# Kernel tuning notes

Hardware: AMD Instinct MI355X
Metric: run time of the kernel (lower is better)

Reference implementation:

```python
import jax, jax.numpy as jnp
import numpy as np

N_GROUP = 8
TOPK_GROUP = 4
TOP_K = 8
ROUTED_SCALING_FACTOR = 2.5


def setup_inputs() -> dict:
    key = jax.random.key(0)
    ks = jax.random.split(key, 6)
    T, H, I, E = 256, 1024, 512, 32
    x = jax.random.normal(ks[0], (T, H), dtype=jnp.float32)
    gate_w = jax.random.normal(ks[1], (H, E), dtype=jnp.float32) * 0.05
    e_score_bias = jax.random.normal(ks[2], (E,), dtype=jnp.float32) * 0.05
    Wg = jax.random.normal(ks[3], (E, H, I), dtype=jnp.float32) * 0.02
    Wu = jax.random.normal(ks[4], (E, H, I), dtype=jnp.float32) * 0.02
    Wd = jax.random.normal(ks[5], (E, I, H), dtype=jnp.float32) * 0.02
    return {"x": x, "gate_w": gate_w, "e_score_bias": e_score_bias,
            "Wg": Wg, "Wu": Wu, "Wd": Wd}


def _route_ds3(x, gate_w, e_score_bias):
    # DeepSeek-V3 group-limited top-k routing (routing_ds3 in source).
    T = x.shape[0]
    E = gate_w.shape[1]
    logits = x @ gate_w                      # [T, E]
    scores = jax.nn.sigmoid(logits)
    scores_for_choice = scores + e_score_bias[None, :]
    gsz = E // N_GROUP
    grouped = scores_for_choice.reshape(T, N_GROUP, gsz)
    # group score = sum of top-2 expert scores in group
    group_scores = jnp.sum(jax.lax.top_k(grouped, 2)[0], axis=-1)     # [T, n_group]
    _, group_idx = jax.lax.top_k(group_scores, TOPK_GROUP)            # [T, topk_group]
    rows = jnp.arange(T)[:, None]
    group_mask = jnp.zeros((T, N_GROUP), scores.dtype).at[rows, group_idx].set(1.0)
    score_mask = jnp.repeat(group_mask, gsz, axis=-1)                 # [T, E]
    masked = jnp.where(score_mask > 0, scores_for_choice, 0.0)
    _, topk_idx = jax.lax.top_k(masked, TOP_K)                        # [T, k]
    topk_w = jnp.take_along_axis(scores, topk_idx, axis=1)            # gather raw scores
    topk_w = topk_w / (jnp.sum(topk_w, axis=-1, keepdims=True) + 1e-20)
    topk_w = topk_w * ROUTED_SCALING_FACTOR
    return topk_idx, topk_w


def reference(x, gate_w, e_score_bias, Wg, Wu, Wd):
    T = x.shape[0]
    E = gate_w.shape[1]
    topk_idx, topk_w = _route_ds3(x, gate_w, e_score_bias)
    # dense [T, E] routing-weight matrix (topk indices are unique per row)
    rows = jnp.arange(T)[:, None]
    rw = jnp.zeros((T, E), x.dtype).at[rows, topk_idx].set(topk_w)
    # expert gated MLP (silu), combined with routing weights
    g = jnp.einsum('th,ehi->tei', x, Wg)      # [T, E, I]
    u = jnp.einsum('th,ehi->tei', x, Wu)
    a = jax.nn.silu(g) * u
    y = jnp.einsum('tei,eih->teh', a, Wd)     # [T, E, H]
    out = jnp.einsum('te,teh->th', rw, y)     # weighted combine
    return out
```

## Files before the change

kernel.cpp:

```cpp
#include <hip/hip_runtime.h>
#include <cstdint>
#include <cmath>

constexpr int TT   = 256;
constexpr int HD   = 1024;
constexpr int IDIM = 512;
constexpr int NE   = 32;
constexpr int NGRP = 8;
constexpr int TKG  = 4;
constexpr int TOPK = 8;
constexpr float RSCALE = 2.5f;

constexpr int NSX  = HD / 32;
constexpr int NSA  = IDIM / 32;
constexpr int SLAB = 16 * 64 * 8;

typedef float    f32x4 __attribute__((ext_vector_type(4)));
typedef _Float16 half8 __attribute__((ext_vector_type(8)));

constexpr size_t WS_CNT   = 0;
constexpr size_t WS_TOK   = 256;
constexpr size_t WS_WL    = WS_TOK   + (size_t)NE * TT * 4;
constexpr size_t WS_TSLOT = WS_WL    + (size_t)NE * TT * 4;
constexpr size_t WS_OFFS  = WS_TSLOT + (size_t)TT * TOPK * 4;
constexpr size_t WS_XE    = WS_OFFS  + 256;
constexpr size_t WS_A     = WS_XE + (size_t)NE * NSX * SLAB * 2;

#define GLOAD16(GP, LP) __builtin_amdgcn_global_load_lds(                      \
    (const __attribute__((address_space(1))) unsigned int*)(GP),               \
    (__attribute__((address_space(3))) unsigned int*)(LP), 16, 0, 0)

#define WAITVM(N) asm volatile("s_waitcnt vmcnt(" #N ")" ::: "memory")

__global__ __launch_bounds__(256) void k_route(
    const float* __restrict__ x, const float* __restrict__ gw,
    const float* __restrict__ bias, int* __restrict__ cnt,
    int* __restrict__ tok, float* __restrict__ wl, int* __restrict__ tslot)
{
    int t = blockIdx.x;
    int tid = threadIdx.x;
    int e2 = (tid & 15) * 2;
    int c  = tid >> 4;
    const float* xr = x + (size_t)t * HD;

    float a0 = 0.f, a1 = 0.f;
    int h0 = c * (HD / 16);
#pragma unroll 8
    for (int h = h0; h < h0 + HD / 16; ++h) {
        float xv = xr[h];
        float2 wv = *(const float2*)&gw[(size_t)h * NE + e2];
        a0 += xv * wv.x;
        a1 += xv * wv.y;
    }

    __shared__ float part[16][NE];
    part[c][e2]     = a0;
    part[c][e2 + 1] = a1;
    __syncthreads();

    __shared__ float sc[NE], sfc[NE];
    if (tid < NE) {
        float s = 0.f;
#pragma unroll
        for (int cc = 0; cc < 16; ++cc) s += part[cc][tid];
        float sig = 1.f / (1.f + expf(-s));
        sc[tid]  = sig;
        sfc[tid] = sig + bias[tid];
    }
    __syncthreads();

    if (tid == 0) {
        float gs[NGRP];
        for (int g = 0; g < NGRP; ++g) {
            float m1 = -3.0e38f, m2 = -3.0e38f;
            for (int j = 0; j < 4; ++j) {
                float v = sfc[4 * g + j];
                if (v > m1) { m2 = m1; m1 = v; } else if (v > m2) m2 = v;
            }
            gs[g] = m1 + m2;
        }
        bool gsel[NGRP];
        for (int g = 0; g < NGRP; ++g) gsel[g] = false;
        for (int r = 0; r < TKG; ++r) {
            int bi = -1; float bv = -3.0e38f;
            for (int g = 0; g < NGRP; ++g)
                if (!gsel[g] && gs[g] > bv) { bv = gs[g]; bi = g; }
            gsel[bi] = true;
        }
        float masked[NE];
        for (int i = 0; i < NE; ++i) masked[i] = gsel[i >> 2] ? sfc[i] : 0.0f;
        int   idx[TOPK]; float wv[TOPK]; float wsum = 0.f;
        for (int r = 0; r < TOPK; ++r) {
            int bi = -1; float bv = -3.0e38f;
            for (int i = 0; i < NE; ++i)
                if (masked[i] > bv) { bv = masked[i]; bi = i; }
            masked[bi] = -3.0e38f;
            idx[r] = bi; wv[r] = sc[bi]; wsum += wv[r];
        }
        float inv = RSCALE / (wsum + 1e-20f);
        for (int r = 0; r < TOPK; ++r) {
            int ee = idx[r];
            int pos = atomicAdd(&cnt[ee], 1);
            tok[(size_t)ee * TT + pos] = t;
            wl [(size_t)ee * TT + pos] = wv[r] * inv;
            tslot[t * TOPK + r] = ee * TT + pos;
        }
    }
}

__global__ __launch_bounds__(64) void k_offs(const int* __restrict__ cnt,
                                             int* __restrict__ offs)
{
    if (threadIdx.x == 0) {
        int s = 0;
        for (int e = 0; e < NE; ++e) { offs[e] = s; s += cnt[e]; }
    }
}

__global__ __launch_bounds__(256) void k_pack(
    const float* __restrict__ x, const int* __restrict__ cnt,
    const int* __restrict__ tok, _Float16* __restrict__ Xe)
{
    int bid  = blockIdx.x;
    int xcd  = bid & 7;
    int slot = bid >> 3;
    int e    = xcd * 4 + (slot & 3);
    int s    = slot >> 2;
    int n_e = cnt[e];
    if (n_e == 0) return;
    int tid = threadIdx.x, w = tid >> 6, lane = tid & 63;
    int m16 = lane & 15, q = lane >> 4;
    _Float16* base = Xe + ((size_t)e * NSX + s) * SLAB;
#pragma unroll
    for (int k = 0; k < 4; ++k) {
        int mt = w + k * 4;
        int slot2 = mt * 16 + m16;
        if (slot2 >= n_e) slot2 = n_e - 1;
        int t = tok[e * TT + slot2];
        const float* src = x + (size_t)t * HD + s * 32 + q * 8;
        f32x4 v0 = *(const f32x4*)src;
        f32x4 v1 = *(const f32x4*)(src + 4);
        half8 h;
        h[0] = (_Float16)v0.x; h[1] = (_Float16)v0.y; h[2] = (_Float16)v0.z; h[3] = (_Float16)v0.w;
        h[4] = (_Float16)v1.x; h[5] = (_Float16)v1.y; h[6] = (_Float16)v1.z; h[7] = (_Float16)v1.w;
        *(half8*)(base + ((size_t)mt * 64 + lane) * 8) = h;
    }
}

__global__ __launch_bounds__(128, 1) void k_gateup(
    const _Float16* __restrict__ Xe, const float* __restrict__ Wg,
    const float* __restrict__ Wu, const int* __restrict__ cnt,
    _Float16* __restrict__ A)
{
    int bid  = blockIdx.x;
    int xcd  = bid & 7;
    int slot = bid >> 3;
    int e    = xcd * 4 + (slot & 3);
    int rest = slot >> 2;
    int ttile = rest & 1;
    int ig    = rest >> 1;
    int n_e = cnt[e];
    if (ttile * 128 >= n_e) return;
    int mtbase = ttile * 8;
    int i0 = ig * 32;
    int tid  = threadIdx.x;
    int w    = tid >> 6;
    int lane = tid & 63;
    int m16 = lane & 15, q = lane >> 4;
    int wcol = w * 16 + m16;

    __shared__ __align__(16) float    LG[5][32][32];
    __shared__ __align__(16) float    LU[5][32][32];
    __shared__ __align__(16) _Float16 LA[5][4096];

    const _Float16* aslab = Xe + (size_t)e * NSX * SLAB + (size_t)mtbase * 512;
    const float* gw0 = Wg + (size_t)e * HD * IDIM + i0;
    const float* uw0 = Wu + (size_t)e * HD * IDIM + i0;

    f32x4 accG[8], accU[8];
#pragma unroll
    for (int mt = 0; mt < 8; ++mt) {
        accG[mt] = (f32x4){0.f, 0.f, 0.f, 0.f};
        accU[mt] = (f32x4){0.f, 0.f, 0.f, 0.f};
    }

#define GU_STAGE(B, KS)                                                        \
    { _Pragma("unroll")                                                        \
      for (int ci = 0; ci < 2; ++ci) {                                         \
        int c    = w * 2 + ci;                                                 \
        int row  = c * 8 + (lane >> 3);                                        \
        int csrc = ((lane & 7) << 2) ^ ((c & 1) << 4);                         \
        const float* gs = gw0 + ((size_t)(KS) * 32 + row) * IDIM + csrc;       \
        const float* us = uw0 + ((size_t)(KS) * 32 + row) * IDIM + csrc;       \
        GLOAD16(gs, &LG[B][c * 8][0]);                                         \
        GLOAD16(us, &LU[B][c * 8][0]);                                         \
      }                                                                        \
      _Pragma("unroll")                                                        \
      for (int i_ = 0; i_ < 4; ++i_) {                                         \
        int off_ = (w * 4 + i_) * 512;                                         \
        const _Float16* as_ = aslab + (size_t)(KS) * SLAB + off_ + lane * 8;   \
        GLOAD16(as_, &LA[B][off_]);                                            \
      } }

#define GU_COMPUTE(B)                                                          \
    { int lc = wcol ^ ((q & 1) << 4);                                          \
      half8 bg, bu;                                                            \
      _Pragma("unroll")                                                        \
      for (int j_ = 0; j_ < 8; ++j_) {                                         \
        bg[j_] = (_Float16)LG[B][q * 8 + j_][lc];                              \
        bu[j_] = (_Float16)LU[B][q * 8 + j_][lc];                              \
      }                                                                        \
      _Pragma("unroll")                                                        \
      for (int mt_ = 0; mt_ < 8; ++mt_) {                                      \
        half8 afr = *(const half8*)&LA[B][mt_ * 512 + lane * 8];               \
        accG[mt_] = __builtin_amdgcn_mfma_f32_16x16x32_f16(afr, bg, accG[mt_], 0, 0, 0); \
        accU[mt_] = __builtin_amdgcn_mfma_f32_16x16x32_f16(afr, bu, accU[mt_], 0, 0, 0); \
      } }

    constexpr int NK = HD / 32;
    GU_STAGE(0, 0) GU_STAGE(1, 1) GU_STAGE(2, 2)

#pragma unroll
    for (int ks = 0; ks < NK; ++ks) {
        if (ks + 3 < NK) GU_STAGE((ks + 3) % 5, ks + 3)
        if      (ks + 4 <= NK) { WAITVM(24); }
        else if (ks + 3 == NK) { WAITVM(16); }
        else if (ks + 2 == NK) { WAITVM(8);  }
        else                   { WAITVM(0);  }
        __builtin_amdgcn_s_barrier();
        __builtin_amdgcn_sched_barrier(0);
        GU_COMPUTE(ks % 5)
    }
#undef GU_STAGE
#undef GU_COMPUTE

    int iyw = ig * 2 + w;
    _Float16* aout = A + ((size_t)e * NSA + (iyw >> 1)) * SLAB;
    int cj   = m16 & 7;
    int lsub = ((iyw * 2 + (m16 >> 3)) & 3) * 16;
#pragma unroll
    for (int mt = 0; mt < 8; ++mt) {
#pragma unroll
        for (int r = 0; r < 4; ++r) {
            float g = accG[mt][r], u = accU[mt][r];
            float a = (g / (1.f + expf(-g))) * u;
            int lp = (q * 4 + r) + lsub;
            aout[((size_t)(mtbase + mt) * 64 + lp) * 8 + cj] = (_Float16)a;
        }
    }
}

__global__ __launch_bounds__(128, 1) void k_down(
    const _Float16* __restrict__ A, const float* __restrict__ Wd,
    const int* __restrict__ cnt, const int* __restrict__ offs,
    const float* __restrict__ wl, float* __restrict__ Y)
{
    int bid  = blockIdx.x;
    int xcd  = bid & 7;
    int slot = bid >> 3;
    int e    = xcd * 4 + (slot & 3);
    int rest = slot >> 2;
    int ttile = rest & 1;
    int hg    = rest >> 1;
    int n_e = cnt[e];
    if (ttile * 128 >= n_e) return;
    int mtbase = ttile * 8;
    int h0 = hg * 32;
    int tid  = threadIdx.x;
    int w    = tid >> 6;
    int lane = tid & 63;
    int m16 = lane & 15, q = lane >> 4;
    int wcol = w * 16 + m16;

    __shared__ __align__(16) float    LD[5][32][32];
    __shared__ __align__(16) _Float16 LA[5][4096];

    const _Float16* aslab = A + (size_t)e * NSA * SLAB + (size_t)mtbase * 512;
    const float* dw0 = Wd + (size_t)e * IDIM * HD + h0;

    f32x4 acc[8];
#pragma unroll
    for (int mt = 0; mt < 8; ++mt) acc[mt] = (f32x4){0.f, 0.f, 0.f, 0.f};

#define DN_STAGE(B, KS)                                                        \
    { _Pragma("unroll")                                                        \
      for (int ci = 0; ci < 2; ++ci) {                                         \
        int c    = w * 2 + ci;                                                 \
        int row  = c * 8 + (lane >> 3);                                        \
        int csrc = ((lane & 7) << 2) ^ ((c & 1) << 4);                         \
        const float* ds = dw0 + ((size_t)(KS) * 32 + row) * HD + csrc;         \
        GLOAD16(ds, &LD[B][c * 8][0]);                                         \
      }                                                                        \
      _Pragma("unroll")                                                        \
      for (int i_ = 0; i_ < 4; ++i_) {                                         \
        int off_ = (w * 4 + i_) * 512;                                         \
        const _Float16* as_ = aslab + (size_t)(KS) * SLAB + off_ + lane * 8;   \
        GLOAD16(as_, &LA[B][off_]);                                            \
      } }

#define DN_COMPUTE(B)                                                          \
    { int lc = wcol ^ ((q & 1) << 4);                                          \
      half8 bd;                                                                \
      _Pragma("unroll")                                                        \
      for (int j_ = 0; j_ < 8; ++j_) bd[j_] = (_Float16)LD[B][q * 8 + j_][lc]; \
      _Pragma("unroll")                                                        \
      for (int mt_ = 0; mt_ < 8; ++mt_) {                                      \
        half8 afr = *(const half8*)&LA[B][mt_ * 512 + lane * 8];               \
        acc[mt_] = __builtin_amdgcn_mfma_f32_16x16x32_f16(afr, bd, acc[mt_], 0, 0, 0); \
      } }

    constexpr int NK = IDIM / 32;
    DN_STAGE(0, 0) DN_STAGE(1, 1) DN_STAGE(2, 2)

#pragma unroll
    for (int ks = 0; ks < NK; ++ks) {
        if (ks + 3 < NK) DN_STAGE((ks + 3) % 5, ks + 3)
        if      (ks + 4 <= NK) { WAITVM(18); }
        else if (ks + 3 == NK) { WAITVM(12); }
        else if (ks + 2 == NK) { WAITVM(6);  }
        else                   { WAITVM(0);  }
        __builtin_amdgcn_s_barrier();
        __builtin_amdgcn_sched_barrier(0);
        DN_COMPUTE(ks % 5)
    }
#undef DN_STAGE
#undef DN_COMPUTE

    int oe = offs[e];
    int col = h0 + w * 16 + m16;
#pragma unroll
    for (int mt = 0; mt < 8; ++mt) {
#pragma unroll
        for (int r = 0; r < 4; ++r) {
            int slot2 = ttile * 128 + mt * 16 + q * 4 + r;
            if (slot2 < n_e) {
                float wt = wl[(size_t)e * TT + slot2];
                Y[(size_t)(oe + slot2) * HD + col] = wt * acc[mt][r];
            }
        }
    }
}

__global__ __launch_bounds__(256) void k_combine(
    const float* __restrict__ Y, const int* __restrict__ tslot,
    const int* __restrict__ offs, float* __restrict__ out)
{
    int t = blockIdx.x, tid = threadIdx.x;
    f32x4 s = (f32x4){0.f, 0.f, 0.f, 0.f};
#pragma unroll
    for (int r = 0; r < TOPK; ++r) {
        int ts  = tslot[t * TOPK + r];
        int e   = ts >> 8;
        int pos = ts & 255;
        const float* yp = Y + (size_t)(offs[e] + pos) * HD + tid * 4;
        f32x4 v = *(const f32x4*)yp;
        s.x += v.x; s.y += v.y; s.z += v.z; s.w += v.w;
    }
    *(f32x4*)&out[(size_t)t * HD + tid * 4] = s;
}

extern "C" void kernel_launch(void* const* d_in, const int* in_sizes, int n_in,
                              void* d_out, int out_size, void* d_ws, size_t ws_size,
                              hipStream_t stream) {
    const float* x    = (const float*)d_in[0];
    const float* gw   = (const float*)d_in[1];
    const float* bias = (const float*)d_in[2];
    const float* Wg   = (const float*)d_in[3];
    const float* Wu   = (const float*)d_in[4];
    const float* Wd   = (const float*)d_in[5];
    float* out = (float*)d_out;

    char* ws = (char*)d_ws;
    int*      cnt   = (int*)(ws + WS_CNT);
    int*      tok   = (int*)(ws + WS_TOK);
    float*    wl    = (float*)(ws + WS_WL);
    int*      tslot = (int*)(ws + WS_TSLOT);
    int*      offs  = (int*)(ws + WS_OFFS);
    _Float16* Xe    = (_Float16*)(ws + WS_XE);
    _Float16* A     = (_Float16*)(ws + WS_A);
    float*    Y     = (float*)(ws + WS_XE);

    hipMemsetAsync(ws, 0, 256, stream);

    k_route<<<TT, 256, 0, stream>>>(x, gw, bias, cnt, tok, wl, tslot);
    k_offs<<<1, 64, 0, stream>>>(cnt, offs);
    k_pack<<<NE * NSX, 256, 0, stream>>>(x, cnt, tok, Xe);
    k_gateup<<<NE * 2 * (IDIM / 32), 128, 0, stream>>>(Xe, Wg, Wu, cnt, A);
    k_down<<<NE * 2 * (HD / 32), 128, 0, stream>>>(A, Wd, cnt, offs, wl, Y);
    k_combine<<<TT, 256, 0, stream>>>(Y, tslot, offs, out);
}
```

Before: 256.6 us.

## Halve GEMM column tiles, split token rows across waves, fold offsets into pack

The gate/up and down kernels now use 16-wide output column tiles, so twice as many blocks launch. The two waves now split the 128 token rows between them instead of splitting columns. The pipeline shrinks from 5 to 3 LDS stages, and MFMA sections are wrapped in s_setprio. The separate single-thread k_offs launch is folded into block 0 of k_pack, which removes one kernel launch. The aim is more parallelism across CUs and lower LDS use per block, at the cost of reading activation tiles twice as often and a shallower prefetch depth.

```diff
diff --git a/kernel.cpp b/kernel.cpp
--- a/kernel.cpp
+++ b/kernel.cpp
@@ -108,27 +108,24 @@
     }
 }
 
-__global__ __launch_bounds__(64) void k_offs(const int* __restrict__ cnt,
-                                             int* __restrict__ offs)
-{
-    if (threadIdx.x == 0) {
+__global__ __launch_bounds__(256) void k_pack(
+    const float* __restrict__ x, const int* __restrict__ cnt,
+    const int* __restrict__ tok, _Float16* __restrict__ Xe,
+    int* __restrict__ offs)
+{
+    int bid  = blockIdx.x;
+    int tid  = threadIdx.x;
+    if (bid == 0 && tid == 0) {
         int s = 0;
         for (int e = 0; e < NE; ++e) { offs[e] = s; s += cnt[e]; }
     }
-}
-
-__global__ __launch_bounds__(256) void k_pack(
-    const float* __restrict__ x, const int* __restrict__ cnt,
-    const int* __restrict__ tok, _Float16* __restrict__ Xe)
-{
-    int bid  = blockIdx.x;
     int xcd  = bid & 7;
     int slot = bid >> 3;
     int e    = xcd * 4 + (slot & 3);
     int s    = slot >> 2;
     int n_e = cnt[e];
     if (n_e == 0) return;
-    int tid = threadIdx.x, w = tid >> 6, lane = tid & 63;
+    int w = tid >> 6, lane = tid & 63;
     int m16 = lane & 15, q = lane >> 4;
     _Float16* base = Xe + ((size_t)e * NSX + s) * SLAB;
 #pragma unroll
@@ -157,95 +154,94 @@
     int slot = bid >> 3;
     int e    = xcd * 4 + (slot & 3);
     int rest = slot >> 2;
-    int ttile = rest & 1;
-    int ig    = rest >> 1;
+    int ig    = rest & 31;
+    int ttile = rest >> 5;
     int n_e = cnt[e];
     if (ttile * 128 >= n_e) return;
     int mtbase = ttile * 8;
-    int i0 = ig * 32;
+    int i0 = ig * 16;
     int tid  = threadIdx.x;
     int w    = tid >> 6;
     int lane = tid & 63;
     int m16 = lane & 15, q = lane >> 4;
-    int wcol = w * 16 + m16;
-
-    __shared__ __align__(16) float    LG[5][32][32];
-    __shared__ __align__(16) float    LU[5][32][32];
-    __shared__ __align__(16) _Float16 LA[5][4096];
+
+    __shared__ __align__(16) float    LG[3][32][16];
+    __shared__ __align__(16) float    LU[3][32][16];
+    __shared__ __align__(16) _Float16 LA[3][4096];
 
     const _Float16* aslab = Xe + (size_t)e * NSX * SLAB + (size_t)mtbase * 512;
     const float* gw0 = Wg + (size_t)e * HD * IDIM + i0;
     const float* uw0 = Wu + (size_t)e * HD * IDIM + i0;
 
-    f32x4 accG[8], accU[8];
-#pragma unroll
-    for (int mt = 0; mt < 8; ++mt) {
+    f32x4 accG[4], accU[4];
+#pragma unroll
+    for (int mt = 0; mt < 4; ++mt) {
         accG[mt] = (f32x4){0.f, 0.f, 0.f, 0.f};
         accU[mt] = (f32x4){0.f, 0.f, 0.f, 0.f};
     }
 
 #define GU_STAGE(B, KS)                                                        \
-    { _Pragma("unroll")                                                        \
-      for (int ci = 0; ci < 2; ++ci) {                                         \
-        int c    = w * 2 + ci;                                                 \
-        int row  = c * 8 + (lane >> 3);                                        \
-        int csrc = ((lane & 7) << 2) ^ ((c & 1) << 4);                         \
-        const float* gs = gw0 + ((size_t)(KS) * 32 + row) * IDIM + csrc;       \
-        const float* us = uw0 + ((size_t)(KS) * 32 + row) * IDIM + csrc;       \
-        GLOAD16(gs, &LG[B][c * 8][0]);                                         \
-        GLOAD16(us, &LU[B][c * 8][0]);                                         \
+    { const float* wp_ = (w == 0) ? gw0 : uw0;                                 \
+      float* lp_ = (w == 0) ? &LG[B][0][0] : &LU[B][0][0];                     \
+      _Pragma("unroll")                                                        \
+      for (int i_ = 0; i_ < 2; ++i_) {                                         \
+        int row_  = i_ * 16 + (lane >> 2);                                     \
+        int csrc_ = ((lane & 3) << 2) ^ (((row_ >> 3) & 3) << 2);              \
+        GLOAD16(wp_ + ((size_t)(KS) * 32 + row_) * IDIM + csrc_,               \
+                lp_ + i_ * 256);                                               \
       }                                                                        \
       _Pragma("unroll")                                                        \
       for (int i_ = 0; i_ < 4; ++i_) {                                         \
         int off_ = (w * 4 + i_) * 512;                                         \
-        const _Float16* as_ = aslab + (size_t)(KS) * SLAB + off_ + lane * 8;   \
-        GLOAD16(as_, &LA[B][off_]);                                            \
+        GLOAD16(aslab + (size_t)(KS) * SLAB + off_ + lane * 8, &LA[B][off_]);  \
       } }
 
 #define GU_COMPUTE(B)                                                          \
-    { int lc = wcol ^ ((q & 1) << 4);                                          \
+    { int lc = m16 ^ (q << 2);                                                 \
       half8 bg, bu;                                                            \
       _Pragma("unroll")                                                        \
       for (int j_ = 0; j_ < 8; ++j_) {                                         \
         bg[j_] = (_Float16)LG[B][q * 8 + j_][lc];                              \
         bu[j_] = (_Float16)LU[B][q * 8 + j_][lc];                              \
       }                                                                        \
-      _Pragma("unroll")                                                        \
-      for (int mt_ = 0; mt_ < 8; ++mt_) {                                      \
-        half8 afr = *(const half8*)&LA[B][mt_ * 512 + lane * 8];               \
+      __builtin_amdgcn_s_setprio(1);                                           \
+      _Pragma("unroll")                                                        \
+      for (int mt_ = 0; mt_ < 4; ++mt_) {                                      \
+        half8 afr = *(const half8*)&LA[B][(w * 4 + mt_) * 512 + lane * 8];     \
         accG[mt_] = __builtin_amdgcn_mfma_f32_16x16x32_f16(afr, bg, accG[mt_], 0, 0, 0); \
         accU[mt_] = __builtin_amdgcn_mfma_f32_16x16x32_f16(afr, bu, accU[mt_], 0, 0, 0); \
-      } }
+      }                                                                        \
+      __builtin_amdgcn_s_setprio(0); }
 
     constexpr int NK = HD / 32;
-    GU_STAGE(0, 0) GU_STAGE(1, 1) GU_STAGE(2, 2)
+    GU_STAGE(0, 0) GU_STAGE(1, 1)
 
 #pragma unroll
     for (int ks = 0; ks < NK; ++ks) {
-        if (ks + 3 < NK) GU_STAGE((ks + 3) % 5, ks + 3)
-        if      (ks + 4 <= NK) { WAITVM(24); }
-        else if (ks + 3 == NK) { WAITVM(16); }
-        else if (ks + 2 == NK) { WAITVM(8);  }
+        __builtin_amdgcn_s_barrier();
+        if (ks + 2 < NK) GU_STAGE((ks + 2) % 3, ks + 2)
+        if      (ks + 2 < NK)  { WAITVM(12); }
+        else if (ks + 1 < NK)  { WAITVM(6);  }
         else                   { WAITVM(0);  }
         __builtin_amdgcn_s_barrier();
         __builtin_amdgcn_sched_barrier(0);
-        GU_COMPUTE(ks % 5)
+        GU_COMPUTE(ks % 3)
     }
 #undef GU_STAGE
 #undef GU_COMPUTE
 
-    int iyw = ig * 2 + w;
+    int iyw = ig;
     _Float16* aout = A + ((size_t)e * NSA + (iyw >> 1)) * SLAB;
     int cj   = m16 & 7;
     int lsub = ((iyw * 2 + (m16 >> 3)) & 3) * 16;
 #pragma unroll
-    for (int mt = 0; mt < 8; ++mt) {
+    for (int mt = 0; mt < 4; ++mt) {
 #pragma unroll
         for (int r = 0; r < 4; ++r) {
             float g = accG[mt][r], u = accU[mt][r];
             float a = (g / (1.f + expf(-g))) * u;
             int lp = (q * 4 + r) + lsub;
-            aout[((size_t)(mtbase + mt) * 64 + lp) * 8 + cj] = (_Float16)a;
+            aout[((size_t)(mtbase + w * 4 + mt) * 64 + lp) * 8 + cj] = (_Float16)a;
         }
     }
 }
@@ -260,79 +256,75 @@
     int slot = bid >> 3;
     int e    = xcd * 4 + (slot & 3);
     int rest = slot >> 2;
-    int ttile = rest & 1;
-    int hg    = rest >> 1;
+    int hg    = rest & 63;
+    int ttile = rest >> 6;
     int n_e = cnt[e];
     if (ttile * 128 >= n_e) return;
     int mtbase = ttile * 8;
-    int h0 = hg * 32;
+    int h0 = hg * 16;
     int tid  = threadIdx.x;
     int w    = tid >> 6;
     int lane = tid & 63;
     int m16 = lane & 15, q = lane >> 4;
-    int wcol = w * 16 + m16;
-
-    __shared__ __align__(16) float    LD[5][32][32];
-    __shared__ __align__(16) _Float16 LA[5][4096];
+
+    __shared__ __align__(16) float    LD[3][32][16];
+    __shared__ __align__(16) _Float16 LA[3][4096];
 
     const _Float16* aslab = A + (size_t)e * NSA * SLAB + (size_t)mtbase * 512;
     const float* dw0 = Wd + (size_t)e * IDIM * HD + h0;
 
-    f32x4 acc[8];
-#pragma unroll
-    for (int mt = 0; mt < 8; ++mt) acc[mt] = (f32x4){0.f, 0.f, 0.f, 0.f};
+    f32x4 acc[4];
+#pragma unroll
+    for (int mt = 0; mt < 4; ++mt) acc[mt] = (f32x4){0.f, 0.f, 0.f, 0.f};
 
 #define DN_STAGE(B, KS)                                                        \
-    { _Pragma("unroll")                                                        \
-      for (int ci = 0; ci < 2; ++ci) {                                         \
-        int c    = w * 2 + ci;                                                 \
-        int row  = c * 8 + (lane >> 3);                                        \
-        int csrc = ((lane & 7) << 2) ^ ((c & 1) << 4);                         \
-        const float* ds = dw0 + ((size_t)(KS) * 32 + row) * HD + csrc;         \
-        GLOAD16(ds, &LD[B][c * 8][0]);                                         \
-      }                                                                        \
+    { int row_  = w * 16 + (lane >> 2);                                        \
+      int csrc_ = ((lane & 3) << 2) ^ (((row_ >> 3) & 3) << 2);                \
+      GLOAD16(dw0 + ((size_t)(KS) * 32 + row_) * HD + csrc_,                   \
+              &LD[B][w * 16][0]);                                              \
       _Pragma("unroll")                                                        \
       for (int i_ = 0; i_ < 4; ++i_) {                                         \
         int off_ = (w * 4 + i_) * 512;                                         \
-        const _Float16* as_ = aslab + (size_t)(KS) * SLAB + off_ + lane * 8;   \
-        GLOAD16(as_, &LA[B][off_]);                                            \
+        GLOAD16(aslab + (size_t)(KS) * SLAB + off_ + lane * 8, &LA[B][off_]);  \
       } }
 
 #define DN_COMPUTE(B)                                                          \
-    { int lc = wcol ^ ((q & 1) << 4);                                          \
+    { int lc = m16 ^ (q << 2);                                                 \
       half8 bd;                                                                \
       _Pragma("unroll")                                                        \
       for (int j_ = 0; j_ < 8; ++j_) bd[j_] = (_Float16)LD[B][q * 8 + j_][lc]; \
-      _Pragma("unroll")                                                        \
-      for (int mt_ = 0; mt_ < 8; ++mt_) {                                      \
-        half8 afr = *(const half8*)&LA[B][mt_ * 512 + lane * 8];               \
+      __builtin_amdgcn_s_setprio(1);                                           \
+      _Pragma("unroll")                                                        \
+      for (int mt_ = 0; mt_ < 4; ++mt_) {                                      \
+        half8 afr = *(const half8*)&LA[B][(w * 4 + mt_) * 512 + lane * 8];     \
         acc[mt_] = __builtin_amdgcn_mfma_f32_16x16x32_f16(afr, bd, acc[mt_], 0, 0, 0); \
-      } }
+      }                                                                        \
+      __builtin_amdgcn_s_setprio(0); }
 
     constexpr int NK = IDIM / 32;
-    DN_STAGE(0, 0) DN_STAGE(1, 1) DN_STAGE(2, 2)
+    DN_STAGE(0, 0) DN_STAGE(1, 1)
 
 #pragma unroll
     for (int ks = 0; ks < NK; ++ks) {
-        if (ks + 3 < NK) DN_STAGE((ks + 3) % 5, ks + 3)
-        if      (ks + 4 <= NK) { WAITVM(18); }
-        else if (ks + 3 == NK) { WAITVM(12); }
-        else if (ks + 2 == NK) { WAITVM(6);  }
+        __builtin_amdgcn_s_barrier();
+        if (ks + 2 < NK) DN_STAGE((ks + 2) % 3, ks + 2)
+        if      (ks + 2 < NK)  { WAITVM(10); }
+        else if (ks + 1 < NK)  { WAITVM(5);  }
         else                   { WAITVM(0);  }
         __builtin_amdgcn_s_barrier();
         __builtin_amdgcn_sched_barrier(0);
-        DN_COMPUTE(ks % 5)
+        DN_COMPUTE(ks % 3)
     }
 #undef DN_STAGE
 #undef DN_COMPUTE
 
     int oe = offs[e];
-    int col = h0 + w * 16 + m16;
-#pragma unroll
-    for (int mt = 0; mt < 8; ++mt) {
+    int col = h0 + m16;
+#pragma unroll
+    for (int mt = 0; mt < 4; ++mt) {
 #pragma unroll
         for (int r = 0; r < 4; ++r) {
-            int slot2 = ttile * 128 + mt * 16 + q * 4 + r;
+            int slot2 = ttile * 128 + (w * 4 + mt) * 16 + q * 4 + r;
             if (slot2 < n_e) {
                 float wt = wl[(size_t)e * TT + slot2];
                 Y[(size_t)(oe + slot2) * HD + col] = wt * acc[mt][r];
@@ -383,9 +375,8 @@
     hipMemsetAsync(ws, 0, 256, stream);
 
     k_route<<<TT, 256, 0, stream>>>(x, gw, bias, cnt, tok, wl, tslot);
-    k_offs<<<1, 64, 0, stream>>>(cnt, offs);
-    k_pack<<<NE * NSX, 256, 0, stream>>>(x, cnt, tok, Xe);
-    k_gateup<<<NE * 2 * (IDIM / 32), 128, 0, stream>>>(Xe, Wg, Wu, cnt, A);
-    k_down<<<NE * 2 * (HD / 32), 128, 0, stream>>>(A, Wd, cnt, offs, wl, Y);
+    k_pack<<<NE * NSX, 256, 0, stream>>>(x, cnt, tok, Xe, offs);
+    k_gateup<<<NE * 2 * (IDIM / 16), 128, 0, stream>>>(Xe, Wg, Wu, cnt, A);
+    k_down<<<NE * 2 * (HD / 16), 128, 0, stream>>>(A, Wd, cnt, offs, wl, Y);
     k_combine<<<TT, 256, 0, stream>>>(Y, tslot, offs, out);
 }
```

After: 267.0 us. 1.04x slower.
